# Performance work log

Measured on AMD Instinct MI355X. Metric: run time of the kernel, lower is better.

The kernel has to match this reference:

```python
import jax, jax.numpy as jnp
import numpy as np

N0, N1, N2 = 200000, 50000, 10000
E0, E1 = 800000, 160000
IN_DIM, H1, H2, EMB = 256, 256, 256, 128


def gcn_layer(h_src, src_idx, dst_idx, n_src, n_dst, W, b):
    # DGL GraphConv, norm='both': D_dst^{-1/2} A D_src^{-1/2} X W + b,
    # degrees clamped to min 1 (allow_zero_in_degree=True -> zero rows stay zero).
    ones = jnp.ones(src_idx.shape[0], dtype=h_src.dtype)
    out_deg = jnp.clip(jax.ops.segment_sum(ones, src_idx, num_segments=n_src), 1.0)
    in_deg = jnp.clip(jax.ops.segment_sum(ones, dst_idx, num_segments=n_dst), 1.0)
    # in_dim >= out_dim here, so DGL multiplies by W first then aggregates;
    # result is identical either way.
    h = (h_src * jax.lax.rsqrt(out_deg)[:, None]) @ W          # [n_src, out]
    agg = jax.ops.segment_sum(h[src_idx], dst_idx, num_segments=n_dst)  # [n_dst, out]
    return agg * jax.lax.rsqrt(in_deg)[:, None] + b


def setup_inputs() -> dict:
    key = jax.random.key(0)
    ks = jax.random.split(key, 10)
    h = jax.random.normal(ks[0], (N0, IN_DIM), dtype=jnp.float32)
    src0 = jax.random.randint(ks[1], (E0,), 0, N0, dtype=jnp.int32)
    dst0 = jax.random.randint(ks[2], (E0,), 0, N1, dtype=jnp.int32)
    src1 = jax.random.randint(ks[3], (E1,), 0, N1, dtype=jnp.int32)
    dst1 = jax.random.randint(ks[4], (E1,), 0, N2, dtype=jnp.int32)
    s1 = 1.0 / np.sqrt(IN_DIM)
    s2 = 1.0 / np.sqrt(H1)
    sp = 1.0 / np.sqrt(H2)
    W1 = jax.random.normal(ks[5], (IN_DIM, H1), dtype=jnp.float32) * s1
    W2 = jax.random.normal(ks[6], (H1, H2), dtype=jnp.float32) * s2
    Wp = jax.random.normal(ks[7], (H2, EMB), dtype=jnp.float32) * sp
    b1 = jnp.zeros((H1,), dtype=jnp.float32)
    b2 = jnp.zeros((H2,), dtype=jnp.float32)
    bp = jnp.zeros((EMB,), dtype=jnp.float32)
    return {"h": h, "src0": src0, "dst0": dst0, "src1": src1, "dst1": dst1,
            "W1": W1, "b1": b1, "W2": W2, "b2": b2, "Wp": Wp, "bp": bp}


def reference(h, src0, dst0, src1, dst1, W1, b1, W2, b2, Wp, bp):
    h = gcn_layer(h, src0, dst0, N0, N1, W1, b1)   # [N1, H1]
    h = gcn_layer(h, src1, dst1, N1, N2, W2, b2)   # [N2, H2]
    return h @ Wp + bp                             # [N2, EMB]
```

## Files before the change

kernel.cpp:

```cpp
#include <hip/hip_runtime.h>
#include <cstddef>

#define N0 200000
#define N1 50000
#define N2 10000
#define E0 800000
#define E1 160000

typedef short bf16x8 __attribute__((ext_vector_type(8)));
typedef float f32x4 __attribute__((ext_vector_type(4)));
typedef unsigned short us8 __attribute__((ext_vector_type(8)));

__device__ __forceinline__ unsigned short f2bf(float f) {
    unsigned int u = __float_as_uint(f);
    unsigned int r = (u + 0x7FFF + ((u >> 16) & 1)) >> 16;
    return (unsigned short)r;
}
__device__ __forceinline__ float bf2f(unsigned short s) {
    return __uint_as_float(((unsigned int)s) << 16);
}

__global__ void pack_all(const float* __restrict__ W1, const float* __restrict__ W2,
                         const float* __restrict__ Wp,
                         unsigned short* __restrict__ W1p, unsigned short* __restrict__ W2p,
                         unsigned short* __restrict__ Wpp) {
    int tid = blockIdx.x * 256 + threadIdx.x;
    if (tid >= 320 * 64) return;
    int lane = tid & 63;
    int tile = tid >> 6;
    const float* W; unsigned short* Bp; int N; int lt;
    if (tile < 128)      { W = W1; Bp = W1p; N = 256; lt = tile; }
    else if (tile < 256) { W = W2; Bp = W2p; N = 256; lt = tile - 128; }
    else                 { W = Wp; Bp = Wpp; N = 128; lt = tile - 256; }
    int s  = lt & 7;
    int ct = lt >> 3;
    int col = ct * 16 + (lane & 15);
    int k0  = s * 32 + (lane >> 4) * 8;
    unsigned short* dst = Bp + ((size_t)lt * 64 + lane) * 8;
#pragma unroll
    for (int j = 0; j < 8; j++) dst[j] = f2bf(W[(size_t)(k0 + j) * N + col]);
}

__global__ void count_all(const int* __restrict__ src0, const int* __restrict__ dst0,
                          const int* __restrict__ src1, const int* __restrict__ dst1,
                          int* __restrict__ cnt_out0, int* __restrict__ cnt_in0,
                          int* __restrict__ cnt_out1, int* __restrict__ cnt_in1,
                          int* __restrict__ rank0, int* __restrict__ rank1) {
    int e = blockIdx.x * 256 + threadIdx.x;
    if (e < E0) {
        atomicAdd(&cnt_out0[src0[e]], 1);
        rank0[e] = atomicAdd(&cnt_in0[dst0[e]], 1);
    } else if (e < E0 + E1) {
        int f = e - E0;
        atomicAdd(&cnt_out1[src1[f]], 1);
        rank1[f] = atomicAdd(&cnt_in1[dst1[f]], 1);
    }
}

__global__ void scales_kernel(const int* __restrict__ cnt, float* __restrict__ rs, int n) {
    int i = blockIdx.x * 256 + threadIdx.x;
    if (i < n) rs[i] = rsqrtf((float)max(cnt[i], 1));
}

__global__ __launch_bounds__(1024) void scan2(const int* __restrict__ cnt_in0, int* __restrict__ rowptr0,
                                              const int* __restrict__ cnt_in1, int* __restrict__ rowptr1) {
    const int* cnt = blockIdx.x ? cnt_in1 : cnt_in0;
    int* rowptr    = blockIdx.x ? rowptr1 : rowptr0;
    const int n    = blockIdx.x ? N2 : N1;
    __shared__ int partial[1024];
    const int t = threadIdx.x;
    const int chunk = (n + 1023) / 1024;
    const int begin = t * chunk;
    const int end = min(begin + chunk, n);
    int sum = 0;
    for (int i = begin; i < end; i++) sum += cnt[i];
    partial[t] = sum;
    __syncthreads();
    for (int off = 1; off < 1024; off <<= 1) {
        int v = (t >= off) ? partial[t - off] : 0;
        __syncthreads();
        partial[t] += v;
        __syncthreads();
    }
    int run = partial[t] - sum;
    for (int i = begin; i < end; i++) {
        rowptr[i] = run;
        run += cnt[i];
    }
    if (t == 1023) rowptr[n] = partial[1023];
}

__global__ void fill_all(const int* __restrict__ src0, const int* __restrict__ dst0,
                         const int* __restrict__ src1, const int* __restrict__ dst1,
                         const int* __restrict__ rank0, const int* __restrict__ rank1,
                         const int* __restrict__ rowptr0, const int* __restrict__ rowptr1,
                         int* __restrict__ csr0, int* __restrict__ csr1) {
    int e = blockIdx.x * 256 + threadIdx.x;
    if (e < E0) {
        csr0[rowptr0[dst0[e]] + rank0[e]] = src0[e];
    } else if (e < E0 + E1) {
        int f = e - E0;
        csr1[rowptr1[dst1[f]] + rank1[f]] = src1[f];
    }
}

template <int NT, bool AF32, bool OBF16>
__global__ __launch_bounds__(256) void gemm_mfma(const void* __restrict__ A_,
                                                 const unsigned short* __restrict__ Bp,
                                                 const float* __restrict__ rs,
                                                 const float* __restrict__ bias,
                                                 void* __restrict__ C_, int M, int N) {
    const int lane = threadIdx.x & 63;
    const int wave = threadIdx.x >> 6;
    const int rowBase = blockIdx.x * 64 + wave * 16;
    const int lm = lane & 15;
    const int quad = lane >> 4;

    f32x4 acc[NT];
#pragma unroll
    for (int ct = 0; ct < NT; ct++) acc[ct] = (f32x4){0.f, 0.f, 0.f, 0.f};

    const int rowA = min(rowBase + lm, M - 1);
    const float* af32 = (const float*)A_ + (size_t)rowA * 256 + quad * 8;
    const unsigned short* abf = (const unsigned short*)A_ + (size_t)rowA * 256 + quad * 8;

#pragma unroll 2
    for (int s = 0; s < 8; s++) {
        bf16x8 afrag;
        if (AF32) {
            float4 x = *(const float4*)(af32 + s * 32);
            float4 y = *(const float4*)(af32 + s * 32 + 4);
            union { unsigned short u[8]; bf16x8 v; } af;
            af.u[0] = f2bf(x.x); af.u[1] = f2bf(x.y); af.u[2] = f2bf(x.z); af.u[3] = f2bf(x.w);
            af.u[4] = f2bf(y.x); af.u[5] = f2bf(y.y); af.u[6] = f2bf(y.z); af.u[7] = f2bf(y.w);
            afrag = af.v;
        } else {
            afrag = *(const bf16x8*)(abf + s * 32);
        }
#pragma unroll
        for (int ct = 0; ct < NT; ct++) {
            bf16x8 bfrag = *(const bf16x8*)(Bp + (((size_t)ct * 8 + s) * 64 + lane) * 8);
            acc[ct] = __builtin_amdgcn_mfma_f32_16x16x32_bf16(afrag, bfrag, acc[ct], 0, 0, 0);
        }
    }

    f32x4 rsv = (f32x4){1.f, 1.f, 1.f, 1.f};
    if (rs) rsv = *(const f32x4*)(rs + rowBase + quad * 4);
#pragma unroll
    for (int ct = 0; ct < NT; ct++) {
        int col = ct * 16 + lm;
        float bv = bias ? bias[col] : 0.0f;
#pragma unroll
        for (int i = 0; i < 4; i++) {
            int row = rowBase + quad * 4 + i;
            if (row < M) {
                float v = acc[ct][i] * rsv[i] + bv;
                if (OBF16) ((unsigned short*)C_)[(size_t)row * N + col] = f2bf(v);
                else       ((float*)C_)[(size_t)row * N + col] = v;
            }
        }
    }
}

__global__ __launch_bounds__(256) void gather_bf16(const unsigned short* __restrict__ Y,
                                                   const int* __restrict__ rowptr,
                                                   const int* __restrict__ csr,
                                                   const float* __restrict__ rs_dst,
                                                   const float* __restrict__ bias,
                                                   unsigned short* __restrict__ outb, int n_dst) {
    int w    = (blockIdx.x * 256 + threadIdx.x) >> 6;
    int lane = threadIdx.x & 63;
    if (w >= n_dst) return;
    int half = lane >> 5;
    int l32  = lane & 31;
    int e   = rowptr[w];
    int end = rowptr[w + 1];
    float acc[8] = {0.f, 0.f, 0.f, 0.f, 0.f, 0.f, 0.f, 0.f};
    for (; e + 7 < end; e += 8) {
        int s0 = csr[e + half];
        int s1 = csr[e + 2 + half];
        int s2 = csr[e + 4 + half];
        int s3 = csr[e + 6 + half];
        us8 v0 = *(const us8*)(Y + (size_t)s0 * 256 + l32 * 8);
        us8 v1 = *(const us8*)(Y + (size_t)s1 * 256 + l32 * 8);
        us8 v2 = *(const us8*)(Y + (size_t)s2 * 256 + l32 * 8);
        us8 v3 = *(const us8*)(Y + (size_t)s3 * 256 + l32 * 8);
#pragma unroll
        for (int j = 0; j < 8; j++)
            acc[j] += (bf2f(v0[j]) + bf2f(v1[j])) + (bf2f(v2[j]) + bf2f(v3[j]));
    }
    for (; e + 1 < end; e += 2) {
        int s0 = csr[e + half];
        us8 v0 = *(const us8*)(Y + (size_t)s0 * 256 + l32 * 8);
#pragma unroll
        for (int j = 0; j < 8; j++) acc[j] += bf2f(v0[j]);
    }
    if (e < end && half == 0) {
        int s0 = csr[e];
        us8 v0 = *(const us8*)(Y + (size_t)s0 * 256 + l32 * 8);
#pragma unroll
        for (int j = 0; j < 8; j++) acc[j] += bf2f(v0[j]);
    }
#pragma unroll
    for (int j = 0; j < 8; j++) acc[j] += __shfl_xor(acc[j], 32);
    if (half == 0) {
        float sd = rs_dst[w];
        f32x4 ba = *(const f32x4*)(bias + l32 * 8);
        f32x4 bb = *(const f32x4*)(bias + l32 * 8 + 4);
        us8 o;
        o[0] = f2bf(acc[0] * sd + ba[0]);
        o[1] = f2bf(acc[1] * sd + ba[1]);
        o[2] = f2bf(acc[2] * sd + ba[2]);
        o[3] = f2bf(acc[3] * sd + ba[3]);
        o[4] = f2bf(acc[4] * sd + bb[0]);
        o[5] = f2bf(acc[5] * sd + bb[1]);
        o[6] = f2bf(acc[6] * sd + bb[2]);
        o[7] = f2bf(acc[7] * sd + bb[3]);
        *(us8*)(outb + (size_t)w * 256 + l32 * 8) = o;
    }
}

extern "C" void kernel_launch(void* const* d_in, const int* in_sizes, int n_in,
                              void* d_out, int out_size, void* d_ws, size_t ws_size,
                              hipStream_t stream) {
    const float* h    = (const float*)d_in[0];
    const int*   src0 = (const int*)d_in[1];
    const int*   dst0 = (const int*)d_in[2];
    const int*   src1 = (const int*)d_in[3];
    const int*   dst1 = (const int*)d_in[4];
    const float* W1   = (const float*)d_in[5];
    const float* b1   = (const float*)d_in[6];
    const float* W2   = (const float*)d_in[7];
    const float* b2   = (const float*)d_in[8];
    const float* Wp   = (const float*)d_in[9];
    const float* bp   = (const float*)d_in[10];
    float* out = (float*)d_out;

    int* ib = (int*)d_ws;
    int* cnt_out0 = ib;
    int* cnt_in0  = cnt_out0 + N0;
    int* cnt_out1 = cnt_in0 + N1;
    int* cnt_in1  = cnt_out1 + N1;
    int* rowptr0  = ib + 310000;
    int* rowptr1  = ib + 360001;
    int* csr0     = ib + 370004;
    int* csr1     = ib + 1170004;
    float* fb = (float*)(ib + 1330004);
    float* rs_out0 = fb;
    float* rs_in0  = fb + 200000;
    float* rs_out1 = fb + 250000;
    float* rs_in1  = fb + 300000;
    unsigned short* wpk = (unsigned short*)(fb + 310000);
    unsigned short* W1p = wpk;
    unsigned short* W2p = wpk + 65536;
    unsigned short* Wpp = wpk + 131072;
    unsigned short* R   = wpk + 163840;
    int* rank0 = (int*)R;
    int* rank1 = rank0 + E0;
    unsigned short* Y1  = R;
    unsigned short* Y2  = R;
    unsigned short* h2b = R + (size_t)N1 * 256;
    unsigned short* h1b = R + (size_t)N0 * 256;

    hipMemsetAsync(cnt_out0, 0, (size_t)310000 * sizeof(int), stream);

    pack_all<<<80, 256, 0, stream>>>(W1, W2, Wp, W1p, W2p, Wpp);

    count_all<<<(E0 + E1 + 255) / 256, 256, 0, stream>>>(src0, dst0, src1, dst1,
                                                         cnt_out0, cnt_in0, cnt_out1, cnt_in1,
                                                         rank0, rank1);

    scales_kernel<<<(310000 + 255) / 256, 256, 0, stream>>>(cnt_out0, rs_out0, 310000);

    scan2<<<2, 1024, 0, stream>>>(cnt_in0, rowptr0, cnt_in1, rowptr1);

    fill_all<<<(E0 + E1 + 255) / 256, 256, 0, stream>>>(src0, dst0, src1, dst1,
                                                        rank0, rank1, rowptr0, rowptr1, csr0, csr1);

    gemm_mfma<16, true, true><<<N0 / 64, 256, 0, stream>>>(h, W1p, rs_out0, nullptr, Y1, N0, 256);

    gather_bf16<<<(N1 + 3) / 4, 256, 0, stream>>>(Y1, rowptr0, csr0, rs_in0, b1, h1b, N1);

    gemm_mfma<16, false, true><<<(N1 + 63) / 64, 256, 0, stream>>>(h1b, W2p, rs_out1, nullptr, Y2, N1, 256);

    gather_bf16<<<(N2 + 3) / 4, 256, 0, stream>>>(Y2, rowptr1, csr1, rs_in1, b2, h2b, N2);

    gemm_mfma<8, false, false><<<(N2 + 63) / 64, 256, 0, stream>>>(h2b, Wpp, nullptr, bp, out, N2, 128);
}
```

Measured before the change: 715.4 us.

## Stage GEMM weight tiles in LDS and use a 2x2 wave tiling

The MFMA GEMM now streams packed weight fragments into shared memory with global_load_lds in two K-phases. Each block covers 128 rows with a 2x2 wave layout, and each wave reuses every B fragment across four 16-row A tiles. The goal is to cut the repeated per-wave global and L2 traffic for weights and raise MFMA work per load. The cost is more accumulator registers, extra barriers, and tighter occupancy from launch bounds of 2 blocks per CU.

```diff
diff --git a/kernel.cpp b/kernel.cpp
--- a/kernel.cpp
+++ b/kernel.cpp
@@ -18,6 +18,12 @@
 }
 __device__ __forceinline__ float bf2f(unsigned short s) {
     return __uint_as_float(((unsigned int)s) << 16);
+}
+
+__device__ __forceinline__ void gload_lds16(const void* g, void* l) {
+    __builtin_amdgcn_global_load_lds(
+        (const __attribute__((address_space(1))) unsigned int*)g,
+        (__attribute__((address_space(3))) unsigned int*)l, 16, 0, 0);
 }
 
 __global__ void pack_all(const float* __restrict__ W1, const float* __restrict__ W2,
@@ -104,59 +110,96 @@
     }
 }
 
-template <int NT, bool AF32, bool OBF16>
-__global__ __launch_bounds__(256) void gemm_mfma(const void* __restrict__ A_,
-                                                 const unsigned short* __restrict__ Bp,
-                                                 const float* __restrict__ rs,
-                                                 const float* __restrict__ bias,
-                                                 void* __restrict__ C_, int M, int N) {
+template <int MREP, int NTT, bool AF32, bool OBF16>
+__global__ __launch_bounds__(256, 2) void gemm_mfma(const void* __restrict__ A_,
+                                                    const unsigned short* __restrict__ Bp,
+                                                    const float* __restrict__ rs,
+                                                    const float* __restrict__ bias,
+                                                    void* __restrict__ C_, int M, int N) {
+    constexpr int NT = NTT / 2;
     const int lane = threadIdx.x & 63;
-    const int wave = threadIdx.x >> 6;
-    const int rowBase = blockIdx.x * 64 + wave * 16;
-    const int lm = lane & 15;
+    const int wid  = threadIdx.x >> 6;
+    const int wr   = wid >> 1;
+    const int wc   = wid & 1;
+    const int lm   = lane & 15;
     const int quad = lane >> 4;
-
-    f32x4 acc[NT];
-#pragma unroll
-    for (int ct = 0; ct < NT; ct++) acc[ct] = (f32x4){0.f, 0.f, 0.f, 0.f};
-
-    const int rowA = min(rowBase + lm, M - 1);
-    const float* af32 = (const float*)A_ + (size_t)rowA * 256 + quad * 8;
-    const unsigned short* abf = (const unsigned short*)A_ + (size_t)rowA * 256 + quad * 8;
-
-#pragma unroll 2
-    for (int s = 0; s < 8; s++) {
-        bf16x8 afrag;
-        if (AF32) {
-            float4 x = *(const float4*)(af32 + s * 32);
-            float4 y = *(const float4*)(af32 + s * 32 + 4);
-            union { unsigned short u[8]; bf16x8 v; } af;
-            af.u[0] = f2bf(x.x); af.u[1] = f2bf(x.y); af.u[2] = f2bf(x.z); af.u[3] = f2bf(x.w);
-            af.u[4] = f2bf(y.x); af.u[5] = f2bf(y.y); af.u[6] = f2bf(y.z); af.u[7] = f2bf(y.w);
-            afrag = af.v;
-        } else {
-            afrag = *(const bf16x8*)(abf + s * 32);
+    const int rowBlk = blockIdx.x * (2 * MREP * 16);
+
+    __shared__ unsigned short Blds[NTT * 2048];
+
+    f32x4 acc[MREP][NT];
+#pragma unroll
+    for (int m = 0; m < MREP; m++)
+#pragma unroll
+        for (int ct = 0; ct < NT; ct++) acc[m][ct] = (f32x4){0.f, 0.f, 0.f, 0.f};
+
+    const float* aF[MREP];
+    const unsigned short* aB[MREP];
+#pragma unroll
+    for (int m = 0; m < MREP; m++) {
+        int r = min(rowBlk + wr * (MREP * 16) + m * 16 + lm, M - 1);
+        if (AF32) aF[m] = (const float*)A_ + (size_t)r * 256 + quad * 8;
+        else      aB[m] = (const unsigned short*)A_ + (size_t)r * 256 + quad * 8;
+    }
+
+#pragma unroll
+    for (int p = 0; p < 2; p++) {
+        if (p) __syncthreads();
+#pragma unroll
+        for (int t = 0; t < NTT; t++) {
+            int tt = wid * NTT + t;
+            int ct = tt >> 2;
+            int s  = p * 4 + (tt & 3);
+            gload_lds16(Bp + (((size_t)ct * 8 + s) * 64 + lane) * 8,
+                        &Blds[(size_t)tt * 512]);
         }
+        __syncthreads();
+
+#pragma unroll
+        for (int sl = 0; sl < 4; sl++) {
+            const int s = p * 4 + sl;
+            bf16x8 af[MREP];
+#pragma unroll
+            for (int m = 0; m < MREP; m++) {
+                if (AF32) {
+                    float4 x = *(const float4*)(aF[m] + s * 32);
+                    float4 y = *(const float4*)(aF[m] + s * 32 + 4);
+                    union { unsigned short u[8]; bf16x8 v; } a;
+                    a.u[0] = f2bf(x.x); a.u[1] = f2bf(x.y); a.u[2] = f2bf(x.z); a.u[3] = f2bf(x.w);
+                    a.u[4] = f2bf(y.x); a.u[5] = f2bf(y.y); a.u[6] = f2bf(y.z); a.u[7] = f2bf(y.w);
+                    af[m] = a.v;
+                } else {
+                    af[m] = *(const bf16x8*)(aB[m] + s * 32);
+                }
+            }
+#pragma unroll
+            for (int ct = 0; ct < NT; ct++) {
+                int ctg = wc * NT + ct;
+                bf16x8 bfrag = *(const bf16x8*)&Blds[((size_t)(ctg * 4 + sl)) * 512 + lane * 8];
+#pragma unroll
+                for (int m = 0; m < MREP; m++)
+                    acc[m][ct] = __builtin_amdgcn_mfma_f32_16x16x32_bf16(af[m], bfrag, acc[m][ct], 0, 0, 0);
+            }
+        }
+    }
+
+#pragma unroll
+    for (int m = 0; m < MREP; m++) {
+        int rowBase = rowBlk + wr * (MREP * 16) + m * 16;
+        f32x4 rsv = (f32x4){1.f, 1.f, 1.f, 1.f};
+        if (rs) rsv = *(const f32x4*)(rs + rowBase + quad * 4);
 #pragma unroll
         for (int ct = 0; ct < NT; ct++) {
-            bf16x8 bfrag = *(const bf16x8*)(Bp + (((size_t)ct * 8 + s) * 64 + lane) * 8);
-            acc[ct] = __builtin_amdgcn_mfma_f32_16x16x32_bf16(afrag, bfrag, acc[ct], 0, 0, 0);
-        }
-    }
-
-    f32x4 rsv = (f32x4){1.f, 1.f, 1.f, 1.f};
-    if (rs) rsv = *(const f32x4*)(rs + rowBase + quad * 4);
-#pragma unroll
-    for (int ct = 0; ct < NT; ct++) {
-        int col = ct * 16 + lm;
-        float bv = bias ? bias[col] : 0.0f;
-#pragma unroll
-        for (int i = 0; i < 4; i++) {
-            int row = rowBase + quad * 4 + i;
-            if (row < M) {
-                float v = acc[ct][i] * rsv[i] + bv;
-                if (OBF16) ((unsigned short*)C_)[(size_t)row * N + col] = f2bf(v);
-                else       ((float*)C_)[(size_t)row * N + col] = v;
+            int col = wc * (NT * 16) + ct * 16 + lm;
+            float bv = bias ? bias[col] : 0.0f;
+#pragma unroll
+            for (int i = 0; i < 4; i++) {
+                int row = rowBase + quad * 4 + i;
+                if (row < M) {
+                    float v = acc[m][ct][i] * rsv[i] + bv;
+                    if (OBF16) ((unsigned short*)C_)[(size_t)row * N + col] = f2bf(v);
+                    else       ((float*)C_)[(size_t)row * N + col] = v;
+                }
             }
         }
     }
@@ -277,13 +320,13 @@
     fill_all<<<(E0 + E1 + 255) / 256, 256, 0, stream>>>(src0, dst0, src1, dst1,
                                                         rank0, rank1, rowptr0, rowptr1, csr0, csr1);
 
-    gemm_mfma<16, true, true><<<N0 / 64, 256, 0, stream>>>(h, W1p, rs_out0, nullptr, Y1, N0, 256);
+    gemm_mfma<4, 16, true, true><<<(N0 + 127) / 128, 256, 0, stream>>>(h, W1p, rs_out0, nullptr, Y1, N0, 256);
 
     gather_bf16<<<(N1 + 3) / 4, 256, 0, stream>>>(Y1, rowptr0, csr0, rs_in0, b1, h1b, N1);
 
-    gemm_mfma<16, false, true><<<(N1 + 63) / 64, 256, 0, stream>>>(h1b, W2p, rs_out1, nullptr, Y2, N1, 256);
+    gemm_mfma<4, 16, false, true><<<(N1 + 127) / 128, 256, 0, stream>>>(h1b, W2p, rs_out1, nullptr, Y2, N1, 256);
 
     gather_bf16<<<(N2 + 3) / 4, 256, 0, stream>>>(Y2, rowptr1, csr1, rs_in1, b2, h2b, N2);
 
-    gemm_mfma<8, false, false><<<(N2 + 63) / 64, 256, 0, stream>>>(h2b, Wpp, nullptr, bp, out, N2, 128);
-}
+    gemm_mfma<2, 8, false, false><<<(N2 + 63) / 64, 256, 0, stream>>>(h2b, Wpp, nullptr, bp, out, N2, 128);
+}
```

Measured after the change: 718.6 us. No clear change (+0.5%).

## Aggregate before transform to avoid GEMM over all source nodes

Applied to the files above, without the earlier changes.

Reorders each GCN layer to aggregate neighbor features first and apply the weight matrix afterwards. Layer one now gathers fp32 input rows scaled by the source norm, then runs a GEMM over N1 rows instead of N0. The next layer's source-norm scaling and the bias are folded into that GEMM's epilogue, and layer two likewise runs its GEMM on N2 rows. This drops the large GEMM over 200k rows and its bf16 intermediate, at the cost of gathering 256-wide fp32 rows, which doubles the bytes per random read in the first gather.

```diff
diff --git a/kernel.cpp b/kernel.cpp
--- a/kernel.cpp
+++ b/kernel.cpp
@@ -104,7 +104,7 @@
     }
 }
 
-template <int NT, bool AF32, bool OBF16>
+template <int NT, bool AF32, bool OBF16, bool BS>
 __global__ __launch_bounds__(256) void gemm_mfma(const void* __restrict__ A_,
                                                  const unsigned short* __restrict__ Bp,
                                                  const float* __restrict__ rs,
@@ -145,7 +145,7 @@
     }
 
     f32x4 rsv = (f32x4){1.f, 1.f, 1.f, 1.f};
-    if (rs) rsv = *(const f32x4*)(rs + rowBase + quad * 4);
+    if (rs) rsv = *(const f32x4*)(rs + min(rowBase + quad * 4, M - 4));
 #pragma unroll
     for (int ct = 0; ct < NT; ct++) {
         int col = ct * 16 + lm;
@@ -154,11 +154,77 @@
         for (int i = 0; i < 4; i++) {
             int row = rowBase + quad * 4 + i;
             if (row < M) {
-                float v = acc[ct][i] * rsv[i] + bv;
+                float v = acc[ct][i];
+                if (BS) { v = (v + bv) * rsv[i]; }
+                else    { v = v * rsv[i] + bv; }
                 if (OBF16) ((unsigned short*)C_)[(size_t)row * N + col] = f2bf(v);
                 else       ((float*)C_)[(size_t)row * N + col] = v;
             }
         }
+    }
+}
+
+__global__ __launch_bounds__(256) void gather_f32(const float* __restrict__ H,
+                                                  const float* __restrict__ rs_src,
+                                                  const int* __restrict__ rowptr,
+                                                  const int* __restrict__ csr,
+                                                  const float* __restrict__ rs_dst,
+                                                  unsigned short* __restrict__ outb, int n_dst) {
+    int w    = (blockIdx.x * 256 + threadIdx.x) >> 6;
+    int lane = threadIdx.x & 63;
+    if (w >= n_dst) return;
+    int half = lane >> 5;
+    int l32  = lane & 31;
+    int e   = rowptr[w];
+    int end = rowptr[w + 1];
+    float acc[8] = {0.f, 0.f, 0.f, 0.f, 0.f, 0.f, 0.f, 0.f};
+    for (; e + 7 < end; e += 8) {
+        int s0 = csr[e + half];
+        int s1 = csr[e + 2 + half];
+        int s2 = csr[e + 4 + half];
+        int s3 = csr[e + 6 + half];
+        float r0 = rs_src[s0], r1 = rs_src[s1], r2 = rs_src[s2], r3 = rs_src[s3];
+        const float* p0 = H + (size_t)s0 * 256 + l32 * 8;
+        const float* p1 = H + (size_t)s1 * 256 + l32 * 8;
+        const float* p2 = H + (size_t)s2 * 256 + l32 * 8;
+        const float* p3 = H + (size_t)s3 * 256 + l32 * 8;
+        float4 x0 = *(const float4*)p0, y0 = *(const float4*)(p0 + 4);
+        float4 x1 = *(const float4*)p1, y1 = *(const float4*)(p1 + 4);
+        float4 x2 = *(const float4*)p2, y2 = *(const float4*)(p2 + 4);
+        float4 x3 = *(const float4*)p3, y3 = *(const float4*)(p3 + 4);
+        acc[0] += x0.x * r0 + x1.x * r1 + x2.x * r2 + x3.x * r3;
+        acc[1] += x0.y * r0 + x1.y * r1 + x2.y * r2 + x3.y * r3;
+        acc[2] += x0.z * r0 + x1.z * r1 + x2.z * r2 + x3.z * r3;
+        acc[3] += x0.w * r0 + x1.w * r1 + x2.w * r2 + x3.w * r3;
+        acc[4] += y0.x * r0 + y1.x * r1 + y2.x * r2 + y3.x * r3;
+        acc[5] += y0.y * r0 + y1.y * r1 + y2.y * r2 + y3.y * r3;
+        acc[6] += y0.z * r0 + y1.z * r1 + y2.z * r2 + y3.z * r3;
+        acc[7] += y0.w * r0 + y1.w * r1 + y2.w * r2 + y3.w * r3;
+    }
+    for (; e + 1 < end; e += 2) {
+        int s0 = csr[e + half];
+        float r0 = rs_src[s0];
+        const float* p0 = H + (size_t)s0 * 256 + l32 * 8;
+        float4 x0 = *(const float4*)p0, y0 = *(const float4*)(p0 + 4);
+        acc[0] += x0.x * r0; acc[1] += x0.y * r0; acc[2] += x0.z * r0; acc[3] += x0.w * r0;
+        acc[4] += y0.x * r0; acc[5] += y0.y * r0; acc[6] += y0.z * r0; acc[7] += y0.w * r0;
+    }
+    if (e < end && half == 0) {
+        int s0 = csr[e];
+        float r0 = rs_src[s0];
+        const float* p0 = H + (size_t)s0 * 256 + l32 * 8;
+        float4 x0 = *(const float4*)p0, y0 = *(const float4*)(p0 + 4);
+        acc[0] += x0.x * r0; acc[1] += x0.y * r0; acc[2] += x0.z * r0; acc[3] += x0.w * r0;
+        acc[4] += y0.x * r0; acc[5] += y0.y * r0; acc[6] += y0.z * r0; acc[7] += y0.w * r0;
+    }
+#pragma unroll
+    for (int j = 0; j < 8; j++) acc[j] += __shfl_xor(acc[j], 32);
+    if (half == 0) {
+        float sd = rs_dst[w];
+        us8 o;
+#pragma unroll
+        for (int j = 0; j < 8; j++) o[j] = f2bf(acc[j] * sd);
+        *(us8*)(outb + (size_t)w * 256 + l32 * 8) = o;
     }
 }
 
@@ -205,17 +271,16 @@
     for (int j = 0; j < 8; j++) acc[j] += __shfl_xor(acc[j], 32);
     if (half == 0) {
         float sd = rs_dst[w];
-        f32x4 ba = *(const f32x4*)(bias + l32 * 8);
-        f32x4 bb = *(const f32x4*)(bias + l32 * 8 + 4);
+        float bj[8] = {0.f, 0.f, 0.f, 0.f, 0.f, 0.f, 0.f, 0.f};
+        if (bias) {
+            f32x4 ba = *(const f32x4*)(bias + l32 * 8);
+            f32x4 bb = *(const f32x4*)(bias + l32 * 8 + 4);
+            bj[0] = ba[0]; bj[1] = ba[1]; bj[2] = ba[2]; bj[3] = ba[3];
+            bj[4] = bb[0]; bj[5] = bb[1]; bj[6] = bb[2]; bj[7] = bb[3];
+        }
         us8 o;
-        o[0] = f2bf(acc[0] * sd + ba[0]);
-        o[1] = f2bf(acc[1] * sd + ba[1]);
-        o[2] = f2bf(acc[2] * sd + ba[2]);
-        o[3] = f2bf(acc[3] * sd + ba[3]);
-        o[4] = f2bf(acc[4] * sd + bb[0]);
-        o[5] = f2bf(acc[5] * sd + bb[1]);
-        o[6] = f2bf(acc[6] * sd + bb[2]);
-        o[7] = f2bf(acc[7] * sd + bb[3]);
+#pragma unroll
+        for (int j = 0; j < 8; j++) o[j] = f2bf(acc[j] * sd + bj[j]);
         *(us8*)(outb + (size_t)w * 256 + l32 * 8) = o;
     }
 }
@@ -254,13 +319,14 @@
     unsigned short* W1p = wpk;
     unsigned short* W2p = wpk + 65536;
     unsigned short* Wpp = wpk + 131072;
-    unsigned short* R   = wpk + 163840;
-    int* rank0 = (int*)R;
+    unsigned short* R1  = wpk + 163840;
+    int* rank0 = (int*)R1;
     int* rank1 = rank0 + E0;
-    unsigned short* Y1  = R;
-    unsigned short* Y2  = R;
-    unsigned short* h2b = R + (size_t)N1 * 256;
-    unsigned short* h1b = R + (size_t)N0 * 256;
+    unsigned short* a0b = R1;
+    unsigned short* a1b = R1;
+    unsigned short* R2  = R1 + (size_t)N1 * 256;
+    unsigned short* t1  = R2;
+    unsigned short* h2b = R2;
 
     hipMemsetAsync(cnt_out0, 0, (size_t)310000 * sizeof(int), stream);
 
@@ -277,13 +343,13 @@
     fill_all<<<(E0 + E1 + 255) / 256, 256, 0, stream>>>(src0, dst0, src1, dst1,
                                                         rank0, rank1, rowptr0, rowptr1, csr0, csr1);
 
-    gemm_mfma<16, true, true><<<N0 / 64, 256, 0, stream>>>(h, W1p, rs_out0, nullptr, Y1, N0, 256);
-
-    gather_bf16<<<(N1 + 3) / 4, 256, 0, stream>>>(Y1, rowptr0, csr0, rs_in0, b1, h1b, N1);
-
-    gemm_mfma<16, false, true><<<(N1 + 63) / 64, 256, 0, stream>>>(h1b, W2p, rs_out1, nullptr, Y2, N1, 256);
-
-    gather_bf16<<<(N2 + 3) / 4, 256, 0, stream>>>(Y2, rowptr1, csr1, rs_in1, b2, h2b, N2);
-
-    gemm_mfma<8, false, false><<<(N2 + 63) / 64, 256, 0, stream>>>(h2b, Wpp, nullptr, bp, out, N2, 128);
-}
+    gather_f32<<<(N1 + 3) / 4, 256, 0, stream>>>(h, rs_out0, rowptr0, csr0, rs_in0, a0b, N1);
+
+    gemm_mfma<16, false, true, true><<<(N1 + 63) / 64, 256, 0, stream>>>(a0b, W1p, rs_out1, b1, t1, N1, 256);
+
+    gather_bf16<<<(N2 + 3) / 4, 256, 0, stream>>>(t1, rowptr1, csr1, rs_in1, nullptr, a1b, N2);
+
+    gemm_mfma<16, false, true, false><<<(N2 + 63) / 64, 256, 0, stream>>>(a1b, W2p, nullptr, b2, h2b, N2, 256);
+
+    gemm_mfma<8, false, false, false><<<(N2 + 63) / 64, 256, 0, stream>>>(h2b, Wpp, nullptr, bp, out, N2, 128);
+}
```

Result: faster. 636.2 us, median of 2 (-11.1%).

## Reorder GCN layers to aggregate before transform, shrinking GEMMs to destination rows

Applied to the files above, without the earlier changes.

Both GCN layers now aggregate first and apply the weight matrix afterwards. A new prescale kernel scales the input features by the out-degree rsqrt and converts them to bf16. The gather then runs on these features, and the GEMMs operate on the smaller destination node sets (50k and 10k rows instead of 200k and 50k). The layer-1 GEMM epilogue folds in bias and the next layer's source scaling. This removes most of the large first-layer GEMM compute, at the cost of an extra elementwise pass and a different rounding order.

```diff
diff --git a/kernel.cpp b/kernel.cpp
--- a/kernel.cpp
+++ b/kernel.cpp
@@ -54,6 +54,24 @@
         int f = e - E0;
         atomicAdd(&cnt_out1[src1[f]], 1);
         rank1[f] = atomicAdd(&cnt_in1[dst1[f]], 1);
+    }
+}
+
+__global__ __launch_bounds__(256) void prescale_bf16(const float* __restrict__ H,
+                                                     const int* __restrict__ cnt_out,
+                                                     unsigned short* __restrict__ hsb) {
+    const long long total = (long long)N0 * 32;
+    const long long stride = (long long)gridDim.x * 256;
+    for (long long g = (long long)blockIdx.x * 256 + threadIdx.x; g < total; g += stride) {
+        int row = (int)(g >> 5);
+        float rs = rsqrtf((float)max(cnt_out[row], 1));
+        const float* p = H + g * 8;
+        float4 x = *(const float4*)p;
+        float4 y = *(const float4*)(p + 4);
+        us8 o;
+        o[0] = f2bf(x.x * rs); o[1] = f2bf(x.y * rs); o[2] = f2bf(x.z * rs); o[3] = f2bf(x.w * rs);
+        o[4] = f2bf(y.x * rs); o[5] = f2bf(y.y * rs); o[6] = f2bf(y.z * rs); o[7] = f2bf(y.w * rs);
+        *(us8*)(hsb + g * 8) = o;
     }
 }
 
@@ -104,7 +122,7 @@
     }
 }
 
-template <int NT, bool AF32, bool OBF16>
+template <int NT, bool AF32, bool OBF16, bool BS>
 __global__ __launch_bounds__(256) void gemm_mfma(const void* __restrict__ A_,
                                                  const unsigned short* __restrict__ Bp,
                                                  const float* __restrict__ rs,
@@ -145,7 +163,7 @@
     }
 
     f32x4 rsv = (f32x4){1.f, 1.f, 1.f, 1.f};
-    if (rs) rsv = *(const f32x4*)(rs + rowBase + quad * 4);
+    if (rs) rsv = *(const f32x4*)(rs + min(rowBase + quad * 4, M - 4));
 #pragma unroll
     for (int ct = 0; ct < NT; ct++) {
         int col = ct * 16 + lm;
@@ -154,7 +172,9 @@
         for (int i = 0; i < 4; i++) {
             int row = rowBase + quad * 4 + i;
             if (row < M) {
-                float v = acc[ct][i] * rsv[i] + bv;
+                float v = acc[ct][i];
+                if (BS) { v = (v + bv) * rsv[i]; }
+                else    { v = v * rsv[i] + bv; }
                 if (OBF16) ((unsigned short*)C_)[(size_t)row * N + col] = f2bf(v);
                 else       ((float*)C_)[(size_t)row * N + col] = v;
             }
@@ -205,17 +225,16 @@
     for (int j = 0; j < 8; j++) acc[j] += __shfl_xor(acc[j], 32);
     if (half == 0) {
         float sd = rs_dst[w];
-        f32x4 ba = *(const f32x4*)(bias + l32 * 8);
-        f32x4 bb = *(const f32x4*)(bias + l32 * 8 + 4);
+        float bj[8] = {0.f, 0.f, 0.f, 0.f, 0.f, 0.f, 0.f, 0.f};
+        if (bias) {
+            f32x4 ba = *(const f32x4*)(bias + l32 * 8);
+            f32x4 bb = *(const f32x4*)(bias + l32 * 8 + 4);
+            bj[0] = ba[0]; bj[1] = ba[1]; bj[2] = ba[2]; bj[3] = ba[3];
+            bj[4] = bb[0]; bj[5] = bb[1]; bj[6] = bb[2]; bj[7] = bb[3];
+        }
         us8 o;
-        o[0] = f2bf(acc[0] * sd + ba[0]);
-        o[1] = f2bf(acc[1] * sd + ba[1]);
-        o[2] = f2bf(acc[2] * sd + ba[2]);
-        o[3] = f2bf(acc[3] * sd + ba[3]);
-        o[4] = f2bf(acc[4] * sd + bb[0]);
-        o[5] = f2bf(acc[5] * sd + bb[1]);
-        o[6] = f2bf(acc[6] * sd + bb[2]);
-        o[7] = f2bf(acc[7] * sd + bb[3]);
+#pragma unroll
+        for (int j = 0; j < 8; j++) o[j] = f2bf(acc[j] * sd + bj[j]);
         *(us8*)(outb + (size_t)w * 256 + l32 * 8) = o;
     }
 }
@@ -254,13 +273,15 @@
     unsigned short* W1p = wpk;
     unsigned short* W2p = wpk + 65536;
     unsigned short* Wpp = wpk + 131072;
-    unsigned short* R   = wpk + 163840;
-    int* rank0 = (int*)R;
+    unsigned short* R1  = wpk + 163840;
+    int* rank0 = (int*)R1;
     int* rank1 = rank0 + E0;
-    unsigned short* Y1  = R;
-    unsigned short* Y2  = R;
-    unsigned short* h2b = R + (size_t)N1 * 256;
-    unsigned short* h1b = R + (size_t)N0 * 256;
+    unsigned short* a0b = R1;
+    unsigned short* a1b = R1;
+    unsigned short* R3  = R1 + (size_t)N1 * 256;
+    unsigned short* hsb = R3;
+    unsigned short* t1  = R3;
+    unsigned short* h2b = R3 + (size_t)N1 * 256;
 
     hipMemsetAsync(cnt_out0, 0, (size_t)310000 * sizeof(int), stream);
 
@@ -270,6 +291,8 @@
                                                          cnt_out0, cnt_in0, cnt_out1, cnt_in1,
                                                          rank0, rank1);
 
+    prescale_bf16<<<2048, 256, 0, stream>>>(h, cnt_out0, hsb);
+
     scales_kernel<<<(310000 + 255) / 256, 256, 0, stream>>>(cnt_out0, rs_out0, 310000);
 
     scan2<<<2, 1024, 0, stream>>>(cnt_in0, rowptr0, cnt_in1, rowptr1);
@@ -277,13 +300,13 @@
     fill_all<<<(E0 + E1 + 255) / 256, 256, 0, stream>>>(src0, dst0, src1, dst1,
                                                         rank0, rank1, rowptr0, rowptr1, csr0, csr1);
 
-    gemm_mfma<16, true, true><<<N0 / 64, 256, 0, stream>>>(h, W1p, rs_out0, nullptr, Y1, N0, 256);
-
-    gather_bf16<<<(N1 + 3) / 4, 256, 0, stream>>>(Y1, rowptr0, csr0, rs_in0, b1, h1b, N1);
-
-    gemm_mfma<16, false, true><<<(N1 + 63) / 64, 256, 0, stream>>>(h1b, W2p, rs_out1, nullptr, Y2, N1, 256);
-
-    gather_bf16<<<(N2 + 3) / 4, 256, 0, stream>>>(Y2, rowptr1, csr1, rs_in1, b2, h2b, N2);
-
-    gemm_mfma<8, false, false><<<(N2 + 63) / 64, 256, 0, stream>>>(h2b, Wpp, nullptr, bp, out, N2, 128);
-}
+    gather_bf16<<<(N1 + 3) / 4, 256, 0, stream>>>(hsb, rowptr0, csr0, rs_in0, nullptr, a0b, N1);
+
+    gemm_mfma<16, false, true, true><<<(N1 + 63) / 64, 256, 0, stream>>>(a0b, W1p, rs_out1, b1, t1, N1, 256);
+
+    gather_bf16<<<(N2 + 3) / 4, 256, 0, stream>>>(t1, rowptr1, csr1, rs_in1, nullptr, a1b, N2);
+
+    gemm_mfma<16, false, true, false><<<(N2 + 63) / 64, 256, 0, stream>>>(a1b, W2p, nullptr, b2, h2b, N2, 256);
+
+    gemm_mfma<8, false, false, false><<<(N2 + 63) / 64, 256, 0, stream>>>(h2b, Wpp, nullptr, bp, out, N2, 128);
+}
```

After: 662.1 us. -7.4%, faster.
